# Optimization experiments

Measured on AMD Instinct MI355X. Metric: run time of the kernel, lower is better.

Reference implementation:

```python
import jax, jax.numpy as jnp
import numpy as np

C0 = 0.28209479177387814
C1 = 0.4886025119029199
C2 = (1.0925484305920792, -1.0925484305920792, 0.31539156525252005,
      -1.0925484305920792, 0.5462742152960396)
EPS = 1e-6


def eval_sh_bases2(d):
    # d: [..., 3] unit directions -> [..., 9] SH basis (degree 2, svox2 convention)
    x, y, z = d[..., 0], d[..., 1], d[..., 2]
    return jnp.stack([
        jnp.full_like(x, C0),
        -C1 * y, C1 * z, -C1 * x,
        C2[0] * x * y, C2[1] * y * z,
        C2[2] * (2.0 * z * z - x * x - y * y),
        C2[3] * x * z, C2[4] * (x * x - y * y),
    ], axis=-1)


def get_sh_vals(xyz, sh_feats, invs, locs):
    # xyz: [N,3]; sh_feats: [J,9]; invs: [J,4,4]; locs: [J,3] -> weights [N,J]
    n = xyz.shape[0]
    xyz_h = jnp.concatenate([xyz, jnp.ones((n, 1), xyz.dtype)], axis=-1)  # [N,4]
    pts = jnp.einsum('jab,nb->jna', invs, xyz_h)[..., :3]  # [J,N,3]
    vd = locs[:, None, :] - pts                             # [J,N,3]
    norm = jnp.linalg.norm(vd, axis=-1)                     # [J,N]
    lengths = jnp.nan_to_num(norm)
    vd = vd / jnp.maximum(norm, 1e-12)[..., None]           # F.normalize
    sh = eval_sh_bases2(vd)                                 # [J,N,9]
    rads = jax.nn.relu(jnp.einsum('jnk,jk->jn', sh, sh_feats) + 0.5)
    rel = jax.nn.relu(1.0 - lengths / jnp.maximum(rads, EPS))
    rel = jnp.where(rads < EPS, 0.0, rel)
    return rel.T  # [N,J]


def weighted_transformation(pts, weights, transforms):
    # pts: [M,3]; weights: [M,J]; transforms: [J,4,4] (already inverse transforms,
    # if_transform_is_inv=True). Linear-blend the matrices and apply.
    wsum = weights.sum(axis=-1, keepdims=True)              # [M,1]
    wn = weights / jnp.maximum(wsum, EPS)
    T = jnp.einsum('mj,jab->mab', wn, transforms)           # [M,4,4]
    p_h = jnp.concatenate([pts, jnp.ones((pts.shape[0], 1), pts.dtype)], axis=-1)
    out = jnp.einsum('mab,mb->ma', T, p_h)[:, :3]
    return jnp.where(wsum > EPS, out, pts)                  # untouched if no weight


def setup_inputs() -> dict:
    key = jax.random.key(0)
    ks = jax.random.split(key, 5)
    B, S, J = 4096, 128, 24
    return {
        'xyz_sampled': jax.random.normal(ks[0], (B, S, 3), jnp.float32),
        'viewdirs': jax.random.normal(ks[1], (B, S, 3), jnp.float32),
        'transforms': jax.random.normal(ks[2], (J, 4, 4), jnp.float32),
        'ray_valid': jnp.ones((B, S), dtype=bool),
        'sh_feats': jax.random.normal(ks[3], (J, 9), jnp.float32),
        'locs': jax.random.normal(ks[4], (J, 3), jnp.float32),
    }


def reference(xyz_sampled, viewdirs, transforms, ray_valid, sh_feats, locs):
    shape = xyz_sampled.shape
    x = xyz_sampled.reshape(-1, 3)
    n = x.shape[0]
    tmp = jnp.concatenate([x, (xyz_sampled - viewdirs).reshape(-1, 3)], axis=0)  # [2N,3]
    w = get_sh_vals(x, sh_feats, transforms, locs)          # [N,J]
    w2 = jnp.concatenate([w, w], axis=0)                    # [2N,J]
    tmp = weighted_transformation(tmp, w2, transforms)      # [2N,3]
    xyz_out = tmp[:n]
    view_out = xyz_out - tmp[n:]
    return xyz_out.reshape(shape), view_out.reshape(shape)
```

## Files before the change

### kernel.cpp

```cpp
#include <hip/hip_runtime.h>

#define EPS 1e-6f
#define J 24

__global__ void fold_kernel(const float* __restrict__ transforms,
                            const float* __restrict__ sh_feats,
                            const float* __restrict__ locs,
                            float* __restrict__ cj)
{
    const int j = threadIdx.x;
    if (j >= J) return;

    float F[9];
    #pragma unroll
    for (int k = 0; k < 9; ++k) F[k] = sh_feats[j * 9 + k];

    const float C0  = 0.28209479177387814f;
    const float C1  = 0.4886025119029199f;
    const float C2a = 1.0925484305920792f;

    const float f0  = C0 * F[0] + 0.5f;
    const float cy  = -C1 * F[1];
    const float cz  =  C1 * F[2];
    const float cx  = -C1 * F[3];
    const float cxy =  C2a * F[4];
    const float cyz = -C2a * F[5];
    const float c6  = 0.31539156525252005f * F[6];
    const float cxz = -C2a * F[7];
    const float c8  = 0.5462742152960396f  * F[8];

    float* s = cj + j * 28;
    #pragma unroll
    for (int k = 0; k < 12; ++k) s[k] = transforms[j * 16 + k];
    s[12] = locs[j * 3 + 0];
    s[13] = locs[j * 3 + 1];
    s[14] = locs[j * 3 + 2];
    s[15] = f0;
    s[16] = cx;  s[17] = cy;  s[18] = cz;
    s[19] = cxy; s[20] = cyz; s[21] = cxz;
    s[22] = c8 - c6;
    s[23] = -c6 - c8;
    s[24] = 2.0f * c6;
    s[25] = 0.f; s[26] = 0.f; s[27] = 0.f;
}

__global__ __launch_bounds__(256, 8) void shcaster_kernel(
    const float* __restrict__ xyz,
    const float* __restrict__ vdir,
    const float* __restrict__ cj,
    float* __restrict__ out,
    int n)
{
    const int i = blockIdx.x * blockDim.x + threadIdx.x;
    if (i >= n) return;

    const float px = xyz[3 * i + 0];
    const float py = xyz[3 * i + 1];
    const float pz = xyz[3 * i + 2];
    const float vx = vdir[3 * i + 0];
    const float vy = vdir[3 * i + 1];
    const float vz = vdir[3 * i + 2];

    float wsum = 0.f;
    float Ta[12];
    #pragma unroll
    for (int k = 0; k < 12; ++k) Ta[k] = 0.f;

    #pragma unroll
    for (int j = 0; j < J; ++j) {
        const float* s = cj + j * 28;

        const float ax = fmaf(s[0], px, fmaf(s[1], py, fmaf(s[2],  pz, s[3])));
        const float ay = fmaf(s[4], px, fmaf(s[5], py, fmaf(s[6],  pz, s[7])));
        const float az = fmaf(s[8], px, fmaf(s[9], py, fmaf(s[10], pz, s[11])));

        const float dx = s[12] - ax;
        const float dy = s[13] - ay;
        const float dz = s[14] - az;
        const float d2 = fmaf(dx, dx, fmaf(dy, dy, dz * dz));

        const float inv_n = __builtin_amdgcn_rsqf(fmaxf(d2, 1e-24f));
        const float len = d2 * inv_n;
        const float nx = dx * inv_n;
        const float ny = dy * inv_n;
        const float nz = dz * inv_n;

        float rads = s[15];
        rads = fmaf(s[16], nx, rads);
        rads = fmaf(s[17], ny, rads);
        rads = fmaf(s[18], nz, rads);
        rads = fmaf(s[19], nx * ny, rads);
        rads = fmaf(s[20], ny * nz, rads);
        rads = fmaf(s[21], nx * nz, rads);
        rads = fmaf(s[22], nx * nx, rads);
        rads = fmaf(s[23], ny * ny, rads);
        rads = fmaf(s[24], nz * nz, rads);
        rads = fmaxf(rads, 0.f);

        float rel = fmaxf(1.f - len * __builtin_amdgcn_rcpf(fmaxf(rads, EPS)), 0.f);
        rel = (rads < EPS) ? 0.f : rel;

        wsum += rel;
        Ta[0]  = fmaf(rel, s[0],  Ta[0]);
        Ta[1]  = fmaf(rel, s[1],  Ta[1]);
        Ta[2]  = fmaf(rel, s[2],  Ta[2]);
        Ta[3]  = fmaf(rel, s[3],  Ta[3]);
        Ta[4]  = fmaf(rel, s[4],  Ta[4]);
        Ta[5]  = fmaf(rel, s[5],  Ta[5]);
        Ta[6]  = fmaf(rel, s[6],  Ta[6]);
        Ta[7]  = fmaf(rel, s[7],  Ta[7]);
        Ta[8]  = fmaf(rel, s[8],  Ta[8]);
        Ta[9]  = fmaf(rel, s[9],  Ta[9]);
        Ta[10] = fmaf(rel, s[10], Ta[10]);
        Ta[11] = fmaf(rel, s[11], Ta[11]);
    }

    const float inv_w = __builtin_amdgcn_rcpf(fmaxf(wsum, EPS));
    const bool valid = wsum > EPS;

    const float axo = fmaf(Ta[0], px, fmaf(Ta[1], py, fmaf(Ta[2],  pz, Ta[3])))  * inv_w;
    const float ayo = fmaf(Ta[4], px, fmaf(Ta[5], py, fmaf(Ta[6],  pz, Ta[7])))  * inv_w;
    const float azo = fmaf(Ta[8], px, fmaf(Ta[9], py, fmaf(Ta[10], pz, Ta[11]))) * inv_w;

    const float qx = px - vx;
    const float qy = py - vy;
    const float qz = pz - vz;
    const float bxo = fmaf(Ta[0], qx, fmaf(Ta[1], qy, fmaf(Ta[2],  qz, Ta[3])))  * inv_w;
    const float byo = fmaf(Ta[4], qx, fmaf(Ta[5], qy, fmaf(Ta[6],  qz, Ta[7])))  * inv_w;
    const float bzo = fmaf(Ta[8], qx, fmaf(Ta[9], qy, fmaf(Ta[10], qz, Ta[11]))) * inv_w;

    const float ox = valid ? axo : px;
    const float oy = valid ? ayo : py;
    const float oz = valid ? azo : pz;
    const float wx = ox - (valid ? bxo : qx);
    const float wy = oy - (valid ? byo : qy);
    const float wz = oz - (valid ? bzo : qz);

    out[3 * i + 0] = ox;
    out[3 * i + 1] = oy;
    out[3 * i + 2] = oz;
    float* out2 = out + (size_t)3 * n;
    out2[3 * i + 0] = wx;
    out2[3 * i + 1] = wy;
    out2[3 * i + 2] = wz;
}

extern "C" void kernel_launch(void* const* d_in, const int* in_sizes, int n_in,
                              void* d_out, int out_size, void* d_ws, size_t ws_size,
                              hipStream_t stream) {
    const int n = (out_size > 0) ? (out_size / 6) : 524288;
    const int big = 3 * n;

    const float* xyz  = nullptr;
    const float* vdir = nullptr;
    const float* trf  = nullptr;
    const float* shf  = nullptr;
    const float* locs = nullptr;
    int bigSeen = 0;
    for (int k = 0; k < n_in; ++k) {
        const int s = in_sizes[k];
        if (s == big) {
            if (bigSeen++ == 0) xyz = (const float*)d_in[k];
            else                vdir = (const float*)d_in[k];
        } else if (s == 384) {
            trf = (const float*)d_in[k];
        } else if (s == 216) {
            shf = (const float*)d_in[k];
        } else if (s == 72) {
            locs = (const float*)d_in[k];
        }
    }
    if (!xyz || !vdir || !trf || !shf || !locs) {
        xyz  = (const float*)d_in[0];
        vdir = (const float*)d_in[1];
        trf  = (const float*)d_in[2];
        shf  = (const float*)d_in[n_in >= 6 ? 4 : 3];
        locs = (const float*)d_in[n_in >= 6 ? 5 : 4];
    }

    float* cj = (float*)d_ws;
    float* out = (float*)d_out;

    fold_kernel<<<1, 64, 0, stream>>>(trf, shf, locs, cj);

    const int block = 256;
    const int grid = (n + block - 1) / block;
    shcaster_kernel<<<grid, block, 0, stream>>>(xyz, vdir, cj, out, n);
}
```

Baseline: 92.09 us.

## Interleave joint pairs and vectorize per-joint math with packed float2 FMAs

The folded per-joint constant table is re-laid out so two joints share each slot, interleaved as float2 pairs. The main loop processes two joints per iteration with 2-wide vector ops, which lets the compiler emit packed FP32 instructions (v_pk_fma_f32 on CDNA) and fetch the constants as 64-bit scalar loads. The aim is to roughly halve the ALU instruction count in this compute-bound kernel. The trade-offs are extra accumulator registers, a final reduction of the two lanes, and a loop that is only partially unrolled.

```diff
diff --git a/kernel.cpp b/kernel.cpp
--- a/kernel.cpp
+++ b/kernel.cpp
@@ -2,6 +2,17 @@
 
 #define EPS 1e-6f
 #define J 24
+#define NPAIR 12
+#define PAIR_STRIDE 56
+
+typedef float v2f __attribute__((ext_vector_type(2)));
+
+__device__ __forceinline__ v2f fma2(v2f a, v2f b, v2f c) {
+    return __builtin_elementwise_fma(a, b, c);
+}
+__device__ __forceinline__ v2f max2(v2f a, v2f b) {
+    return __builtin_elementwise_max(a, b);
+}
 
 __global__ void fold_kernel(const float* __restrict__ transforms,
                             const float* __restrict__ sh_feats,
@@ -29,19 +40,22 @@
     const float cxz = -C2a * F[7];
     const float c8  = 0.5462742152960396f  * F[8];
 
-    float* s = cj + j * 28;
-    #pragma unroll
-    for (int k = 0; k < 12; ++k) s[k] = transforms[j * 16 + k];
-    s[12] = locs[j * 3 + 0];
-    s[13] = locs[j * 3 + 1];
-    s[14] = locs[j * 3 + 2];
-    s[15] = f0;
-    s[16] = cx;  s[17] = cy;  s[18] = cz;
-    s[19] = cxy; s[20] = cyz; s[21] = cxz;
-    s[22] = c8 - c6;
-    s[23] = -c6 - c8;
-    s[24] = 2.0f * c6;
-    s[25] = 0.f; s[26] = 0.f; s[27] = 0.f;
+    float vals[25];
+    #pragma unroll
+    for (int k = 0; k < 12; ++k) vals[k] = transforms[j * 16 + k];
+    vals[12] = locs[j * 3 + 0];
+    vals[13] = locs[j * 3 + 1];
+    vals[14] = locs[j * 3 + 2];
+    vals[15] = f0;
+    vals[16] = cx;  vals[17] = cy;  vals[18] = cz;
+    vals[19] = cxy; vals[20] = cyz; vals[21] = cxz;
+    vals[22] = c8 - c6;
+    vals[23] = -c6 - c8;
+    vals[24] = 2.0f * c6;
+
+    float* base = cj + (j >> 1) * PAIR_STRIDE + (j & 1);
+    #pragma unroll
+    for (int k = 0; k < 25; ++k) base[2 * k] = vals[k];
 }
 
 __global__ __launch_bounds__(256, 8) void shcaster_kernel(
@@ -61,59 +75,74 @@
     const float vy = vdir[3 * i + 1];
     const float vz = vdir[3 * i + 2];
 
-    float wsum = 0.f;
+    const v2f px2 = {px, px};
+    const v2f py2 = {py, py};
+    const v2f pz2 = {pz, pz};
+    const v2f one2  = {1.f, 1.f};
+    const v2f zero2 = {0.f, 0.f};
+
+    v2f wsum2 = zero2;
+    v2f Ta2[12];
+    #pragma unroll
+    for (int k = 0; k < 12; ++k) Ta2[k] = zero2;
+
+    #pragma unroll 4
+    for (int pp = 0; pp < NPAIR; ++pp) {
+        const v2f* s = (const v2f*)(cj + pp * PAIR_STRIDE);
+
+        const v2f ax = fma2(s[0], px2, fma2(s[1], py2, fma2(s[2],  pz2, s[3])));
+        const v2f ay = fma2(s[4], px2, fma2(s[5], py2, fma2(s[6],  pz2, s[7])));
+        const v2f az = fma2(s[8], px2, fma2(s[9], py2, fma2(s[10], pz2, s[11])));
+
+        const v2f dx = s[12] - ax;
+        const v2f dy = s[13] - ay;
+        const v2f dz = s[14] - az;
+        v2f d2 = fma2(dx, dx, fma2(dy, dy, dz * dz));
+        d2 = max2(d2, (v2f){1e-24f, 1e-24f});
+
+        const v2f inv = {__builtin_amdgcn_rsqf(d2.x), __builtin_amdgcn_rsqf(d2.y)};
+        const v2f len = d2 * inv;
+        const v2f nx = dx * inv;
+        const v2f ny = dy * inv;
+        const v2f nz = dz * inv;
+
+        v2f rads = s[15];
+        rads = fma2(s[16], nx, rads);
+        rads = fma2(s[17], ny, rads);
+        rads = fma2(s[18], nz, rads);
+        rads = fma2(s[19], nx * ny, rads);
+        rads = fma2(s[20], ny * nz, rads);
+        rads = fma2(s[21], nx * nz, rads);
+        rads = fma2(s[22], nx * nx, rads);
+        rads = fma2(s[23], ny * ny, rads);
+        rads = fma2(s[24], nz * nz, rads);
+        rads = max2(rads, zero2);
+
+        const v2f rc = {__builtin_amdgcn_rcpf(fmaxf(rads.x, EPS)),
+                        __builtin_amdgcn_rcpf(fmaxf(rads.y, EPS))};
+        v2f rel = max2(fma2(-len, rc, one2), zero2);
+        rel.x = (rads.x < EPS) ? 0.f : rel.x;
+        rel.y = (rads.y < EPS) ? 0.f : rel.y;
+
+        wsum2 += rel;
+        Ta2[0]  = fma2(rel, s[0],  Ta2[0]);
+        Ta2[1]  = fma2(rel, s[1],  Ta2[1]);
+        Ta2[2]  = fma2(rel, s[2],  Ta2[2]);
+        Ta2[3]  = fma2(rel, s[3],  Ta2[3]);
+        Ta2[4]  = fma2(rel, s[4],  Ta2[4]);
+        Ta2[5]  = fma2(rel, s[5],  Ta2[5]);
+        Ta2[6]  = fma2(rel, s[6],  Ta2[6]);
+        Ta2[7]  = fma2(rel, s[7],  Ta2[7]);
+        Ta2[8]  = fma2(rel, s[8],  Ta2[8]);
+        Ta2[9]  = fma2(rel, s[9],  Ta2[9]);
+        Ta2[10] = fma2(rel, s[10], Ta2[10]);
+        Ta2[11] = fma2(rel, s[11], Ta2[11]);
+    }
+
+    const float wsum = wsum2.x + wsum2.y;
     float Ta[12];
     #pragma unroll
-    for (int k = 0; k < 12; ++k) Ta[k] = 0.f;
-
-    #pragma unroll
-    for (int j = 0; j < J; ++j) {
-        const float* s = cj + j * 28;
-
-        const float ax = fmaf(s[0], px, fmaf(s[1], py, fmaf(s[2],  pz, s[3])));
-        const float ay = fmaf(s[4], px, fmaf(s[5], py, fmaf(s[6],  pz, s[7])));
-        const float az = fmaf(s[8], px, fmaf(s[9], py, fmaf(s[10], pz, s[11])));
-
-        const float dx = s[12] - ax;
-        const float dy = s[13] - ay;
-        const float dz = s[14] - az;
-        const float d2 = fmaf(dx, dx, fmaf(dy, dy, dz * dz));
-
-        const float inv_n = __builtin_amdgcn_rsqf(fmaxf(d2, 1e-24f));
-        const float len = d2 * inv_n;
-        const float nx = dx * inv_n;
-        const float ny = dy * inv_n;
-        const float nz = dz * inv_n;
-
-        float rads = s[15];
-        rads = fmaf(s[16], nx, rads);
-        rads = fmaf(s[17], ny, rads);
-        rads = fmaf(s[18], nz, rads);
-        rads = fmaf(s[19], nx * ny, rads);
-        rads = fmaf(s[20], ny * nz, rads);
-        rads = fmaf(s[21], nx * nz, rads);
-        rads = fmaf(s[22], nx * nx, rads);
-        rads = fmaf(s[23], ny * ny, rads);
-        rads = fmaf(s[24], nz * nz, rads);
-        rads = fmaxf(rads, 0.f);
-
-        float rel = fmaxf(1.f - len * __builtin_amdgcn_rcpf(fmaxf(rads, EPS)), 0.f);
-        rel = (rads < EPS) ? 0.f : rel;
-
-        wsum += rel;
-        Ta[0]  = fmaf(rel, s[0],  Ta[0]);
-        Ta[1]  = fmaf(rel, s[1],  Ta[1]);
-        Ta[2]  = fmaf(rel, s[2],  Ta[2]);
-        Ta[3]  = fmaf(rel, s[3],  Ta[3]);
-        Ta[4]  = fmaf(rel, s[4],  Ta[4]);
-        Ta[5]  = fmaf(rel, s[5],  Ta[5]);
-        Ta[6]  = fmaf(rel, s[6],  Ta[6]);
-        Ta[7]  = fmaf(rel, s[7],  Ta[7]);
-        Ta[8]  = fmaf(rel, s[8],  Ta[8]);
-        Ta[9]  = fmaf(rel, s[9],  Ta[9]);
-        Ta[10] = fmaf(rel, s[10], Ta[10]);
-        Ta[11] = fmaf(rel, s[11], Ta[11]);
-    }
+    for (int k = 0; k < 12; ++k) Ta[k] = Ta2[k].x + Ta2[k].y;
 
     const float inv_w = __builtin_amdgcn_rcpf(fmaxf(wsum, EPS));
     const bool valid = wsum > EPS;
```

Measured after the change: 89.75 us. 2.5% less time.
